# Kernel optimization log

Measured on AMD Instinct MI355X. Metric: run time of the kernel, lower is better.

## Reference

```python
import jax, jax.numpy as jnp
import numpy as np

N_EMBD = 2048
N_HEAD = 32
N_GROUPS = 8
HEAD_DIM = N_EMBD // N_HEAD
Q_PER_KV = N_HEAD // N_GROUPS
QKV_DIM = (Q_PER_KV + 2) * N_GROUPS * HEAD_DIM


def apply_rope(x, cos, sin):
    # x: [B, nH, T, hd]; cos/sin: [T, rot//2]
    B, nH, T, hd = x.shape
    rot = min(sin.shape[1] * 2, hd)
    half = rot // 2
    x_rot, x_pass = x[..., :rot], x[..., rot:]
    c = cos[:T, :half][None, None]  # [1,1,T,half]
    s = sin[:T, :half][None, None]
    x1, x2 = x_rot[..., :half], x_rot[..., half:]
    x1_ = x1 * c - x2 * s
    x2_ = x2 * c + x1 * s
    return jnp.concatenate([x1_, x2_, x_pass], axis=-1)


def setup_inputs() -> dict:
    key = jax.random.key(0)
    k1, k2, k3, k4, k5 = jax.random.split(key, 5)
    B, T = 2, 2048
    x = jax.random.normal(k1, (B, T, N_EMBD), dtype=jnp.float32)
    cos = jax.random.uniform(k2, (T, HEAD_DIM // 2), dtype=jnp.float32)
    sin = jax.random.uniform(k3, (T, HEAD_DIM // 2), dtype=jnp.float32)
    attn_w = jax.random.normal(k4, (QKV_DIM, N_EMBD), dtype=jnp.float32) * (1.0 / np.sqrt(N_EMBD))
    proj_w = jax.random.normal(k5, (N_EMBD, N_EMBD), dtype=jnp.float32) * (1.0 / np.sqrt(N_EMBD))
    return {"x": x, "cos": cos, "sin": sin, "attn_w": attn_w, "proj_w": proj_w}


def reference(x, cos, sin, attn_w, proj_w):
    B, T, E = x.shape
    qkv = jnp.einsum('bte,fe->btf', x, attn_w)  # [B,T,QKV_DIM]
    qkv = qkv.reshape(B, T, N_GROUPS, Q_PER_KV + 2, HEAD_DIM)
    q = qkv[:, :, :, :Q_PER_KV].reshape(B, T, N_HEAD, HEAD_DIM)
    k = qkv[:, :, :, Q_PER_KV]      # [B,T,G,hd]
    v = qkv[:, :, :, Q_PER_KV + 1]  # [B,T,G,hd]
    # [B, heads, T, hd] layout; GQA repeat_interleave of K/V to full head count
    q = q.transpose(0, 2, 1, 3)
    k = jnp.repeat(k.transpose(0, 2, 1, 3), Q_PER_KV, axis=1)
    v = jnp.repeat(v.transpose(0, 2, 1, 3), Q_PER_KV, axis=1)
    q = apply_rope(q, cos, sin)
    k = apply_rope(k, cos, sin)
    scale = 1.0 / np.sqrt(HEAD_DIM)
    att = jax.nn.softmax(jnp.einsum('bhqd,bhkd->bhqk', q, k) * scale, axis=-1)
    out = jnp.einsum('bhqk,bhkd->bhqd', att, v)  # [B,nH,T,hd]
    out = out.transpose(0, 2, 1, 3).reshape(B, T, N_HEAD * HEAD_DIM)
    return jnp.einsum('bte,fe->btf', out, proj_w)
```

## Files before the change

### kernel.cpp

```cpp
#include <hip/hip_runtime.h>

typedef unsigned short u16;
typedef unsigned int u32;
typedef __bf16 bf16x8 __attribute__((ext_vector_type(8)));
typedef float f32x4 __attribute__((ext_vector_type(4)));
typedef float f32x16 __attribute__((ext_vector_type(16)));
typedef unsigned int u32x4 __attribute__((ext_vector_type(4)));

__device__ __forceinline__ u16 f2bf(float f) {
    u32 u = __builtin_bit_cast(u32, f);
    u32 r = u + 0x7FFFu + ((u >> 16) & 1u);
    return (u16)(r >> 16);
}
__device__ __forceinline__ u32 pack_bf16(float v0, float v1) {
    u32 a = __builtin_bit_cast(u32, v0) + 0x8000u;
    u32 b = __builtin_bit_cast(u32, v1) + 0x8000u;
    return __builtin_amdgcn_perm(b, a, 0x07060302u);
}
__device__ __forceinline__ u32 cvtpk(float lo, float hi) {
    u32 r;
    asm("v_cvt_pk_bf16_f32 %0, %1, %2" : "=v"(r) : "v"(lo), "v"(hi));
    return r;
}
__device__ __forceinline__ void plswap(u32& a, u32& b) {
    asm("v_permlane32_swap_b32 %0, %1" : "+v"(a), "+v"(b));
}
__device__ __forceinline__ void gload16(const u16* g, u16* l) {
    __builtin_amdgcn_global_load_lds(
        (const __attribute__((address_space(1))) u32*)g,
        (__attribute__((address_space(3))) u32*)l, 16, 0, 0);
}

#define QSCALE 0.18033688011111793f

__global__ __launch_bounds__(256) void cvt3_kernel(const float* __restrict__ a, u16* __restrict__ ao,
                                                   const float* __restrict__ b, u16* __restrict__ bo,
                                                   const float* __restrict__ c, u16* __restrict__ co) {
    int i = blockIdx.x * 256 + threadIdx.x;
    const float* src; u16* dst; int idx;
    if (i < 2097152)       { src = a; dst = ao; idx = i; }
    else if (i < 3670016)  { src = b; dst = bo; idx = i - 2097152; }
    else                   { src = c; dst = co; idx = i - 3670016; }
    float4 f = reinterpret_cast<const float4*>(src)[idx];
    u32 lo = (u32)f2bf(f.x) | ((u32)f2bf(f.y) << 16);
    u32 hi = (u32)f2bf(f.z) | ((u32)f2bf(f.w) << 16);
    reinterpret_cast<uint2*>(dst)[idx] = make_uint2(lo, hi);
}

__global__ __launch_bounds__(512, 2) void gemm_qkv(const u16* __restrict__ A,
                                                   const u16* __restrict__ Bw,
                                                   const float* __restrict__ cosb,
                                                   const float* __restrict__ sinb,
                                                   u16* __restrict__ Qo,
                                                   u16* __restrict__ Ko,
                                                   u16* __restrict__ Vt) {
    __shared__ __align__(16) u16 As[2 * 2 * 128 * 64];
    __shared__ __align__(16) u16 Bs[2 * 2 * 128 * 64];
    const int tid = threadIdx.x;
    const int w = tid >> 6, lane = tid & 63;
    const int quad = lane >> 4, l15 = lane & 15;
    const int wr = w >> 2, wc = w & 3;
    const int m0 = blockIdx.x * 256, n0 = blockIdx.y * 256;
    const int K = 2048;
    const int rsub = lane >> 3;
    const int csrc = (lane & 7) ^ rsub;
    const int sx = (l15 & 7) << 3;
    const int c0 = (quad * 8) ^ sx;
    const int c1 = (32 + quad * 8) ^ sx;

    f32x4 acc[8][4];
#pragma unroll
    for (int a = 0; a < 8; a++)
#pragma unroll
        for (int b = 0; b < 4; b++) acc[a][b] = (f32x4){0.f, 0.f, 0.f, 0.f};

    auto stage = [&](const u16* g, int row0, int kk, u16* lds) {
#pragma unroll
        for (int i = 0; i < 2; i++)
            gload16(g + (size_t)(row0 + (i * 8 + w) * 8 + rsub) * K + kk + csrc * 8,
                    lds + (i * 8 + w) * 512);
    };

    stage(A,  m0,       0, &As[0]);
    stage(A,  m0 + 128, 0, &As[8192]);
    stage(Bw, n0,       0, &Bs[0]);
    stage(Bw, n0 + 128, 0, &Bs[8192]);
    asm volatile("s_waitcnt vmcnt(0)" ::: "memory");
    __builtin_amdgcn_s_barrier();

    for (int j = 0; j < 32; ++j) {
        const int cur = j & 1;
        const u16* Ab = &As[cur * 16384 + wr * 8192];
        const u16* Bb = &Bs[cur * 16384 + (wc >> 1) * 8192 + (wc & 1) * 4096];
        u16* Asn = &As[(cur ^ 1) * 16384];
        u16* Bsn = &Bs[(cur ^ 1) * 16384];
        const int kk2 = (j + 1) * 64;
        bf16x8 af[4][2];
#pragma unroll
        for (int q = 0; q < 4; ++q) {
            const int qm = q >> 1, qn = q & 1;
            if (qn == 0) {
#pragma unroll
                for (int fm = 0; fm < 4; fm++) {
                    af[fm][0] = *reinterpret_cast<const bf16x8*>(&Ab[(qm * 64 + fm * 16 + l15) * 64 + c0]);
                    af[fm][1] = *reinterpret_cast<const bf16x8*>(&Ab[(qm * 64 + fm * 16 + l15) * 64 + c1]);
                }
            }
            bf16x8 bfv[2][2];
#pragma unroll
            for (int fn = 0; fn < 2; fn++) {
                bfv[fn][0] = *reinterpret_cast<const bf16x8*>(&Bb[(qn * 32 + fn * 16 + l15) * 64 + c0]);
                bfv[fn][1] = *reinterpret_cast<const bf16x8*>(&Bb[(qn * 32 + fn * 16 + l15) * 64 + c1]);
            }
            if (j < 31) {
                if (q == 0)      { stage(A,  m0,       kk2, Asn); stage(A,  m0 + 128, kk2, Asn + 8192); }
                else if (q == 1) { stage(Bw, n0,       kk2, Bsn); stage(Bw, n0 + 128, kk2, Bsn + 8192); }
            }
            __builtin_amdgcn_s_barrier();
            __builtin_amdgcn_s_setprio(1);
#pragma unroll
            for (int fm = 0; fm < 4; fm++)
#pragma unroll
                for (int fn = 0; fn < 2; fn++) {
                    acc[qm * 4 + fm][qn * 2 + fn] = __builtin_amdgcn_mfma_f32_16x16x32_bf16(
                        af[fm][0], bfv[fn][0], acc[qm * 4 + fm][qn * 2 + fn], 0, 0, 0);
                    acc[qm * 4 + fm][qn * 2 + fn] = __builtin_amdgcn_mfma_f32_16x16x32_bf16(
                        af[fm][1], bfv[fn][1], acc[qm * 4 + fm][qn * 2 + fn], 0, 0, 0);
                }
            __builtin_amdgcn_s_setprio(0);
            if (q == 3 && j < 31) asm volatile("s_waitcnt vmcnt(0)" ::: "memory");
            __builtin_amdgcn_s_barrier();
        }
    }

    const int nw0 = n0 + wc * 64;
    const int G = nw0 / 384;
    const int slot = (nw0 % 384) / 64;
    const int bb = m0 >> 11;
    const int tb0 = (m0 & 2047) + wr * 128 + quad * 4;
    if (slot == 5) {
        u16* vbase = Vt + ((size_t)(bb * 8 + G) * 64) * 2048;
#pragma unroll
        for (int fm = 0; fm < 8; fm++) {
            const int trow = tb0 + fm * 16;
#pragma unroll
            for (int fn = 0; fn < 4; fn++) {
                const int d = fn * 16 + l15;
                uint2 pk;
                pk.x = pack_bf16(acc[fm][fn][0], acc[fm][fn][1]);
                pk.y = pack_bf16(acc[fm][fn][2], acc[fm][fn][3]);
                *reinterpret_cast<uint2*>(vbase + (size_t)d * 2048 + trow) = pk;
            }
        }
    } else {
        const float sc = (slot < 4) ? QSCALE : 1.0f;
        u16* obase = (slot < 4)
            ? Qo + ((size_t)(bb * 32 + G * 4 + slot) * 2048) * 64
            : Ko + ((size_t)(bb * 8 + G) * 2048) * 64;
#pragma unroll
        for (int fm = 0; fm < 8; fm++) {
#pragma unroll
            for (int i = 0; i < 4; i++) {
                const int t = tb0 + fm * 16 + i;
#pragma unroll
                for (int fn = 0; fn < 2; fn++) {
                    const int dh = fn * 16 + l15;
                    float c = cosb[t * 32 + dh], s = sinb[t * 32 + dh];
                    float x1 = acc[fm][fn][i], x2 = acc[fm][fn + 2][i];
                    obase[(size_t)t * 64 + dh]      = f2bf((x1 * c - x2 * s) * sc);
                    obase[(size_t)t * 64 + dh + 32] = f2bf((x2 * c + x1 * s) * sc);
                }
            }
        }
    }
}

__global__ __launch_bounds__(256) void gemm_bt(const u16* __restrict__ A,
                                               const u16* __restrict__ Bw,
                                               float* __restrict__ Cf,
                                               int M, int N, int K) {
    __shared__ __align__(16) u16 As[2 * 128 * 32];
    __shared__ __align__(16) u16 Bs[2 * 128 * 32];
    const int tid = threadIdx.x;
    const int wave = tid >> 6, lane = tid & 63, quad = lane >> 4, l15 = lane & 15;
    const int wm = wave >> 1, wn = wave & 1;
    const int m0 = blockIdx.x * 128, n0 = blockIdx.y * 128;
    const int lrow = lane >> 2, lcol = (lane & 3) * 8;
    f32x4 acc[4][4];
#pragma unroll
    for (int a = 0; a < 4; a++)
#pragma unroll
        for (int b = 0; b < 4; b++) acc[a][b] = (f32x4){0.f, 0.f, 0.f, 0.f};
    for (int kk = 0; kk < K; kk += 64) {
        __syncthreads();
#pragma unroll
        for (int p = 0; p < 2; p++)
#pragma unroll
            for (int c = 0; c < 2; c++) {
                const int rA = wave * 32 + c * 16;
                gload16(A  + (size_t)(m0 + rA + lrow) * K + kk + p * 32 + lcol,
                        &As[p * 4096 + rA * 32]);
                gload16(Bw + (size_t)(n0 + rA + lrow) * K + kk + p * 32 + lcol,
                        &Bs[p * 4096 + rA * 32]);
            }
        __syncthreads();
#pragma unroll
        for (int p = 0; p < 2; p++) {
            bf16x8 af[4], bfr[4];
#pragma unroll
            for (int t = 0; t < 4; t++) {
                af[t]  = *reinterpret_cast<const bf16x8*>(
                    &As[p * 4096 + (wm * 64 + t * 16 + l15) * 32 + quad * 8]);
                bfr[t] = *reinterpret_cast<const bf16x8*>(
                    &Bs[p * 4096 + (wn * 64 + t * 16 + l15) * 32 + quad * 8]);
            }
#pragma unroll
            for (int tm = 0; tm < 4; tm++)
#pragma unroll
                for (int tn = 0; tn < 4; tn++)
                    acc[tm][tn] = __builtin_amdgcn_mfma_f32_16x16x32_bf16(af[tm], bfr[tn], acc[tm][tn], 0, 0, 0);
        }
    }
#pragma unroll
    for (int tm = 0; tm < 4; tm++) {
        const int r0 = m0 + wm * 64 + tm * 16 + quad * 4;
#pragma unroll
        for (int tn = 0; tn < 4; tn++) {
            const int c = n0 + wn * 64 + tn * 16 + l15;
#pragma unroll
            for (int i = 0; i < 4; i++) Cf[(size_t)(r0 + i) * N + c] = acc[tm][tn][i];
        }
    }
}

__global__ __launch_bounds__(256, 4) void attn(const u16* __restrict__ Q,
                                               const u16* __restrict__ Kg,
                                               const u16* __restrict__ Vt,
                                               u16* __restrict__ O) {
    __shared__ __align__(16) u16 Ks[2 * 4096];
    __shared__ __align__(16) u16 Vts[2 * 4096];
    const int tid = threadIdx.x, w = tid >> 6, lane = tid & 63;
    const int half = lane >> 5, l31 = lane & 31;
    const int q0 = blockIdx.x * 128;
    const int h = blockIdx.y, b = blockIdx.z, g = h >> 2;
    const u16* qb = Q + (((size_t)(b * 32 + h)) * 2048 + q0) * 64;
    const u16* kb = Kg + ((size_t)(b * 8 + g)) * 2048 * 64;
    const u16* vb = Vt + ((size_t)(b * 8 + g)) * 64 * 2048;
    const int frow = l31;
    const int fcol = half * 8;

#pragma unroll
    for (int ks = 0; ks < 4; ks++)
        gload16(qb + (size_t)(w * 32 + frow) * 64 + ks * 16 + fcol,
                Ks + (w * 4 + ks) * 512);
    __syncthreads();
    bf16x8 qf[4];
#pragma unroll
    for (int ks = 0; ks < 4; ks++)
        qf[ks] = *reinterpret_cast<const bf16x8*>(&Ks[(w * 4 + ks) * 512 + lane * 8]);
    __syncthreads();

    f32x16 Oa[2];
#pragma unroll
    for (int t = 0; t < 2; t++)
#pragma unroll
        for (int i = 0; i < 16; i++) Oa[t][i] = 0.f;
    float lsum = 0.f;

    auto stage_kv = [&](int kk, int bsel) {
        u16* kd = Ks + bsel * 4096;
        u16* vd = Vts + bsel * 4096;
#pragma unroll
        for (int i = 0; i < 2; i++) {
            const int s = w * 2 + i;
            const int st = s >> 2, sk = s & 3;
            gload16(kb + (size_t)(kk + st * 32 + frow) * 64 + sk * 16 + fcol,
                    kd + s * 512);
            gload16(vb + (size_t)(st * 32 + frow) * 2048 + kk + sk * 16 + fcol,
                    vd + s * 512);
        }
    };

    stage_kv(0, 0);
    __syncthreads();

    for (int t = 0; t < 32; t++) {
        if (t < 31) stage_kv((t + 1) * 64, (t + 1) & 1);
        const u16* Kb = Ks + (t & 1) * 4096;
        const u16* Vb = Vts + (t & 1) * 4096;

        float ps = 0.f;
        u32 pw[4][4];
#pragma unroll
        for (int kt = 0; kt < 2; kt++) {
            f32x16 S;
#pragma unroll
            for (int i = 0; i < 16; i++) S[i] = 0.f;
            __builtin_amdgcn_s_setprio(1);
#pragma unroll
            for (int ks = 0; ks < 4; ks++) {
                bf16x8 kf = *reinterpret_cast<const bf16x8*>(
                    &Kb[(kt * 4 + ks) * 512 + lane * 8]);
                S = __builtin_amdgcn_mfma_f32_32x32x16_bf16(kf, qf[ks], S, 0, 0, 0);
            }
            __builtin_amdgcn_s_setprio(0);
            float pe[16];
#pragma unroll
            for (int r = 0; r < 16; r++) pe[r] = __builtin_amdgcn_exp2f(S[r]);
#pragma unroll
            for (int r = 0; r < 4; r++)
                ps += (pe[r * 4 + 0] + pe[r * 4 + 1]) + (pe[r * 4 + 2] + pe[r * 4 + 3]);
#pragma unroll
            for (int j = 0; j < 2; j++) {
                u32 X0 = cvtpk(pe[j * 8 + 0], pe[j * 8 + 1]);
                u32 Y0 = cvtpk(pe[j * 8 + 4], pe[j * 8 + 5]);
                u32 X1 = cvtpk(pe[j * 8 + 2], pe[j * 8 + 3]);
                u32 Y1 = cvtpk(pe[j * 8 + 6], pe[j * 8 + 7]);
                plswap(X0, Y0);
                plswap(X1, Y1);
                const int ks2 = kt * 2 + j;
                pw[ks2][0] = X0; pw[ks2][1] = X1; pw[ks2][2] = Y0; pw[ks2][3] = Y1;
            }
        }
        lsum += ps;
        __builtin_amdgcn_s_setprio(1);
#pragma unroll
        for (int ks2 = 0; ks2 < 4; ks2++) {
            u32x4 pv = (u32x4){pw[ks2][0], pw[ks2][1], pw[ks2][2], pw[ks2][3]};
            bf16x8 pf = __builtin_bit_cast(bf16x8, pv);
#pragma unroll
            for (int dt = 0; dt < 2; dt++) {
                bf16x8 vf = *reinterpret_cast<const bf16x8*>(
                    &Vb[(dt * 4 + ks2) * 512 + lane * 8]);
                Oa[dt] = __builtin_amdgcn_mfma_f32_32x32x16_bf16(vf, pf, Oa[dt], 0, 0, 0);
            }
        }
        __builtin_amdgcn_s_setprio(0);
        __syncthreads();
    }
    float lt = lsum + __shfl_xor(lsum, 32);
    float linv = 1.f / lt;
    const int t = q0 + w * 32 + l31;
    u16* orow = O + ((size_t)(b * 2048 + t)) * 2048 + h * 64;
#pragma unroll
    for (int dt = 0; dt < 2; dt++)
#pragma unroll
        for (int gr = 0; gr < 4; gr++) {
            uint2 pk;
            pk.x = pack_bf16(Oa[dt][gr * 4 + 0] * linv, Oa[dt][gr * 4 + 1] * linv);
            pk.y = pack_bf16(Oa[dt][gr * 4 + 2] * linv, Oa[dt][gr * 4 + 3] * linv);
            *reinterpret_cast<uint2*>(orow + dt * 32 + 8 * gr + 4 * half) = pk;
        }
}

extern "C" void kernel_launch(void* const* d_in, const int* in_sizes, int n_in,
                              void* d_out, int out_size, void* d_ws, size_t ws_size,
                              hipStream_t stream) {
    const float* x      = (const float*)d_in[0];
    const float* cosb   = (const float*)d_in[1];
    const float* sinb   = (const float*)d_in[2];
    const float* attn_w = (const float*)d_in[3];
    const float* proj_w = (const float*)d_in[4];
    float* out = (float*)d_out;

    u16* xb  = (u16*)d_ws;
    u16* w1b = xb  + (size_t)4096 * 2048;
    u16* w2b = w1b + (size_t)3072 * 2048;
    u16* qo  = w2b + (size_t)2048 * 2048;
    u16* ko  = qo  + (size_t)2 * 32 * 2048 * 64;
    u16* vt  = ko  + (size_t)2 * 8 * 2048 * 64;
    u16* ao  = xb;

    cvt3_kernel<<<18432, 256, 0, stream>>>(x, xb, attn_w, w1b, proj_w, w2b);
    gemm_qkv<<<dim3(16, 12), 512, 0, stream>>>(xb, w1b, cosb, sinb, qo, ko, vt);
    attn<<<dim3(16, 32, 2), 256, 0, stream>>>(qo, ko, vt, ao);
    gemm_bt<<<dim3(32, 16), 256, 0, stream>>>(ao, w2b, out, 4096, 2048, 2048);
}
```

Measured before the change: 312.2 us.

## Store Q/K/V in fragment-tiled layout so attention loads are contiguous

The QKV GEMM epilogue now writes Q, K and V^T directly in a pre-swizzled, fragment-ordered tile layout that matches the attention kernel's MFMA operand order. The attention kernel then stages each 16-byte-per-lane chunk from contiguous global memory instead of doing strided row gathers. This targets the scattered, poorly coalesced global reads in the attention loads. The trade-off is that the epilogue stores become more scattered, especially the per-element Q/K stores.

```diff
diff --git a/kernel.cpp b/kernel.cpp
--- a/kernel.cpp
+++ b/kernel.cpp
@@ -32,6 +32,7 @@
 }
 
 #define QSCALE 0.18033688011111793f
+
 
 __global__ __launch_bounds__(256) void cvt3_kernel(const float* __restrict__ a, u16* __restrict__ ao,
                                                    const float* __restrict__ b, u16* __restrict__ bo,
@@ -139,36 +140,40 @@
     const int bb = m0 >> 11;
     const int tb0 = (m0 & 2047) + wr * 128 + quad * 4;
     if (slot == 5) {
-        u16* vbase = Vt + ((size_t)(bb * 8 + G) * 64) * 2048;
+        u16* vbase = Vt + ((size_t)(bb * 8 + G)) * 131072;
+        const int half_v = quad >> 1, jb = (quad & 1) * 4;
 #pragma unroll
         for (int fm = 0; fm < 8; fm++) {
             const int trow = tb0 + fm * 16;
+            const int sb = (trow >> 6) * 4096 + ((trow >> 4) & 3) * 512 + half_v * 256 + jb;
 #pragma unroll
             for (int fn = 0; fn < 4; fn++) {
-                const int d = fn * 16 + l15;
+                const int dt = fn >> 1, dl = (fn & 1) * 16 + l15;
                 uint2 pk;
                 pk.x = pack_bf16(acc[fm][fn][0], acc[fm][fn][1]);
                 pk.y = pack_bf16(acc[fm][fn][2], acc[fm][fn][3]);
-                *reinterpret_cast<uint2*>(vbase + (size_t)d * 2048 + trow) = pk;
+                *reinterpret_cast<uint2*>(vbase + sb + dt * 2048 + dl * 8) = pk;
             }
         }
     } else {
         const float sc = (slot < 4) ? QSCALE : 1.0f;
         u16* obase = (slot < 4)
-            ? Qo + ((size_t)(bb * 32 + G * 4 + slot) * 2048) * 64
-            : Ko + ((size_t)(bb * 8 + G) * 2048) * 64;
+            ? Qo + ((size_t)(bb * 32 + G * 4 + slot)) * 131072
+            : Ko + ((size_t)(bb * 8 + G)) * 131072;
+        const int laneoff = (l15 >> 3) * 256 + (l15 & 7);
 #pragma unroll
         for (int fm = 0; fm < 8; fm++) {
 #pragma unroll
             for (int i = 0; i < 4; i++) {
                 const int t = tb0 + fm * 16 + i;
+                const int tb = (t >> 5) * 2048 + (t & 31) * 8 + laneoff;
 #pragma unroll
                 for (int fn = 0; fn < 2; fn++) {
                     const int dh = fn * 16 + l15;
                     float c = cosb[t * 32 + dh], s = sinb[t * 32 + dh];
                     float x1 = acc[fm][fn][i], x2 = acc[fm][fn + 2][i];
-                    obase[(size_t)t * 64 + dh]      = f2bf((x1 * c - x2 * s) * sc);
-                    obase[(size_t)t * 64 + dh + 32] = f2bf((x2 * c + x1 * s) * sc);
+                    obase[tb + fn * 512]       = f2bf((x1 * c - x2 * s) * sc);
+                    obase[tb + (fn + 2) * 512] = f2bf((x2 * c + x1 * s) * sc);
                 }
             }
         }
@@ -243,15 +248,14 @@
     const int half = lane >> 5, l31 = lane & 31;
     const int q0 = blockIdx.x * 128;
     const int h = blockIdx.y, b = blockIdx.z, g = h >> 2;
-    const u16* qb = Q + (((size_t)(b * 32 + h)) * 2048 + q0) * 64;
-    const u16* kb = Kg + ((size_t)(b * 8 + g)) * 2048 * 64;
-    const u16* vb = Vt + ((size_t)(b * 8 + g)) * 64 * 2048;
-    const int frow = l31;
-    const int fcol = half * 8;
-
+    const u16* qfb = Q + ((size_t)(b * 32 + h)) * 131072;
+    const u16* kfb = Kg + ((size_t)(b * 8 + g)) * 131072;
+    const u16* vfb = Vt + ((size_t)(b * 8 + g)) * 131072;
+
+    const int Tq = (q0 >> 6) + (w >> 1);
 #pragma unroll
     for (int ks = 0; ks < 4; ks++)
-        gload16(qb + (size_t)(w * 32 + frow) * 64 + ks * 16 + fcol,
+        gload16(qfb + ((size_t)((Tq * 8 + (w & 1) * 4 + ks) * 64) + lane) * 8,
                 Ks + (w * 4 + ks) * 512);
     __syncthreads();
     bf16x8 qf[4];
@@ -267,17 +271,14 @@
         for (int i = 0; i < 16; i++) Oa[t][i] = 0.f;
     float lsum = 0.f;
 
-    auto stage_kv = [&](int kk, int bsel) {
+    auto stage_kv = [&](int T, int bsel) {
         u16* kd = Ks + bsel * 4096;
         u16* vd = Vts + bsel * 4096;
 #pragma unroll
         for (int i = 0; i < 2; i++) {
             const int s = w * 2 + i;
-            const int st = s >> 2, sk = s & 3;
-            gload16(kb + (size_t)(kk + st * 32 + frow) * 64 + sk * 16 + fcol,
-                    kd + s * 512);
-            gload16(vb + (size_t)(st * 32 + frow) * 2048 + kk + sk * 16 + fcol,
-                    vd + s * 512);
+            gload16(kfb + ((size_t)((T * 8 + s) * 64) + lane) * 8, kd + s * 512);
+            gload16(vfb + ((size_t)((T * 8 + s) * 64) + lane) * 8, vd + s * 512);
         }
     };
 
@@ -285,7 +286,7 @@
     __syncthreads();
 
     for (int t = 0; t < 32; t++) {
-        if (t < 31) stage_kv((t + 1) * 64, (t + 1) & 1);
+        if (t < 31) stage_kv(t + 1, (t + 1) & 1);
         const u16* Kb = Ks + (t & 1) * 4096;
         const u16* Vb = Vts + (t & 1) * 4096;
 
```

Result: no change. 307.3 us (-1.6%).
